# Performance work log

Hardware: AMD Instinct MI355X
Metric: run time of the kernel (lower is better)

## Reference

```python
import jax, jax.numpy as jnp
import numpy as np

N_VERTS = 100000
N_FACES = 200000
C = 512


def setup_inputs() -> dict:
    key = jax.random.key(0)
    ks = jax.random.split(key, 12)
    x = jax.random.normal(ks[0], (1, N_VERTS, C), dtype=jnp.float32) * 0.1
    verts = jax.random.normal(ks[1], (N_VERTS, 3), dtype=jnp.float32)
    faces = jax.random.randint(ks[2], (N_FACES, 3), 0, N_VERTS, dtype=jnp.int32)
    def lin(k, fan_in, fan_out):
        return jax.random.normal(k, (fan_in, fan_out), dtype=jnp.float32) / np.sqrt(fan_in)
    return {
        "x": x, "verts": verts, "faces": faces,
        "W1": lin(ks[3], C, C),    "b1": jnp.zeros((C,), jnp.float32),
        "W2": lin(ks[4], C, 512),  "b2": jnp.zeros((512,), jnp.float32),
        "W3": lin(ks[5], 512, 256),"b3": jnp.zeros((256,), jnp.float32),
        "W4": lin(ks[6], 256, 12), "b4": jnp.zeros((12,), jnp.float32),
    }


def special_procrustes(M):
    # roma.special_procrustes: nearest rotation in SO(3) to M, batched [F,3,3]
    U, S, Vh = jnp.linalg.svd(M)
    det = jnp.linalg.det(jnp.matmul(U, Vh))  # [F]
    D = jnp.stack([jnp.ones_like(det), jnp.ones_like(det), det], axis=-1)  # [F,3]
    return jnp.matmul(U * D[:, None, :], Vh)


def reference(x, verts, faces, W1, b1, W2, b2, W3, b3, W4, b4):
    N = verts.shape[0]
    F = faces.shape[0]
    # prism base: gather 3 vertex positions per face -> [F,3,3]
    prism_base = verts[faces]
    # gather features of the 3 face vertices and mean over them -> [F,C]
    feat = x[0][faces].mean(axis=1)
    # mlp_refine
    h = jax.nn.relu(feat @ W1 + b1)
    h = jax.nn.relu(h @ W2 + b2)
    h = jax.nn.relu(h @ W3 + b3)
    out = h @ W4 + b4  # [F,12]
    # batched 3x3 Procrustes rotation + translation
    rotations = special_procrustes(out[:, :9].reshape(F, 3, 3))
    translations = out[:, 9:]  # [F,3]
    transformed_prism = jnp.matmul(prism_base, rotations) + translations[:, None, :]  # [F,3,3]
    # scatter-add back to vertices with per-vertex face-count normalization
    flat_idx = faces.reshape(-1)  # [3F]
    summed = jax.ops.segment_sum(transformed_prism.reshape(-1, 3), flat_idx, num_segments=N)
    counts = jax.ops.segment_sum(jnp.ones((3 * F,), jnp.float32), flat_idx, num_segments=N)
    features = summed / jnp.clip(counts, 1.0)[:, None]  # [N,3]
    return features[None], transformed_prism, rotations
```

## Files before the change

### kernel.cpp

```cpp
#include <hip/hip_runtime.h>
#include <stdint.h>

typedef __attribute__((ext_vector_type(8))) short short8;
typedef __attribute__((ext_vector_type(4))) float f32x4;
typedef __attribute__((ext_vector_type(4))) unsigned short u16x4;

__device__ __forceinline__ unsigned short f2bf(float x) {
    union { float f; uint32_t u; } v; v.f = x;
    uint32_t u = v.u;
    uint32_t r = (u + 0x7FFFu + ((u >> 16) & 1u)) >> 16;
    return (unsigned short)r;
}
__device__ __forceinline__ float bf2f(unsigned short h) {
    union { uint32_t u; float f; } v; v.u = ((uint32_t)h) << 16;
    return v.f;
}
__device__ __forceinline__ void splitT(float f, unsigned short& hi, unsigned short& lo) {
    union { float f; uint32_t u; } a; a.f = f;
    hi = (unsigned short)(a.u >> 16);
    union { uint32_t u; float f; } b; b.u = a.u & 0xFFFF0000u;
    union { float f; uint32_t u; } c; c.f = f - b.f;
    lo = (unsigned short)(c.u >> 16);
}

__device__ __forceinline__ void gld_lds16(const void* g, void* s) {
    __builtin_amdgcn_global_load_lds(
        (const __attribute__((address_space(1))) void*)(uintptr_t)g,
        (__attribute__((address_space(3))) void*)(uint32_t)(uintptr_t)s,
        16, 0, 0);
}

__device__ __forceinline__ f32x4 mfma16(short8 a, short8 b, f32x4 c) {
    return __builtin_amdgcn_mfma_f32_16x16x32_bf16(a, b, c, 0, 0, 0);
}

__global__ void zero_kernel(float* __restrict__ sums, float* __restrict__ counts, int nverts) {
    int t = blockIdx.x * 256 + threadIdx.x;
    if (t < nverts * 3) sums[t] = 0.0f;
    if (t < nverts)     counts[t] = 0.0f;
}

__global__ void prep_weights(const float* __restrict__ W1, const float* __restrict__ W2,
                             const float* __restrict__ W3,
                             unsigned short* __restrict__ w1h, unsigned short* __restrict__ w1l,
                             unsigned short* __restrict__ w2h, unsigned short* __restrict__ w2l,
                             unsigned short* __restrict__ w3h, unsigned short* __restrict__ w3l) {
    int t = blockIdx.x * 256 + threadIdx.x;
    float v; unsigned short *ph, *pl; size_t o;
    if (t < 262144) {
        int k = t >> 9, n = t & 511;
        v = W1[t]; o = (size_t)n * 512 + k; ph = w1h; pl = w1l;
    } else if (t < 524288) {
        int u = t - 262144; int k = u >> 9, n = u & 511;
        v = W2[u]; o = (size_t)n * 512 + k; ph = w2h; pl = w2l;
    } else if (t < 655360) {
        int u = t - 524288; int k = u >> 8, n = u & 255;
        v = W3[u]; o = (size_t)n * 512 + k; ph = w3h; pl = w3l;
    } else return;
    unsigned short hi = f2bf(v);
    unsigned short lo = f2bf(v - bf2f(hi));
    ph[o] = hi; pl[o] = lo;
}

__global__ void gather_mean(const float* __restrict__ x, const int* __restrict__ faces,
                            unsigned short* __restrict__ Fhi, unsigned short* __restrict__ Flo,
                            int fbase, int fcount, int mrows) {
    int t = blockIdx.x * 256 + threadIdx.x;
    if (t >= (mrows << 7)) return;
    int r = t >> 7;
    int c = (t & 127) << 2;
    f32x4 m = {0.f, 0.f, 0.f, 0.f};
    if (r < fcount) {
        int f = fbase + r;
        int i0 = faces[3 * f], i1 = faces[3 * f + 1], i2 = faces[3 * f + 2];
        f32x4 a = *(const f32x4*)(x + (size_t)i0 * 512 + c);
        f32x4 b = *(const f32x4*)(x + (size_t)i1 * 512 + c);
        f32x4 d = *(const f32x4*)(x + (size_t)i2 * 512 + c);
        m = (a + b + d) * (1.0f / 3.0f);
    }
    u16x4 hv, lv;
#pragma unroll
    for (int j = 0; j < 4; ++j) {
        unsigned short hi = f2bf(m[j]);
        hv[j] = hi;
        lv[j] = f2bf(m[j] - bf2f(hi));
    }
    *(u16x4*)(Fhi + (size_t)r * 512 + c) = hv;
    *(u16x4*)(Flo + (size_t)r * 512 + c) = lv;
}

template<int OUT>
__global__ __launch_bounds__(256, 2)
void gemm_pipe(const unsigned short* __restrict__ Ahi, const unsigned short* __restrict__ Alo,
               const unsigned short* __restrict__ Bhi, const unsigned short* __restrict__ Blo,
               const float* __restrict__ bias,
               void* __restrict__ Out0, unsigned short* __restrict__ Olo,
               int N, int K, int nt) {
    __shared__ __align__(16) unsigned short sm[2][4][128 * 32];

    const int tid  = threadIdx.x;
    const int lane = tid & 63;
    const int w    = tid >> 6;
    const int wr = w >> 1, wc = w & 1;

    const int nwg  = gridDim.x;
    const int orig = blockIdx.x;
    const int q = nwg >> 3, r8 = nwg & 7;
    const int xcd = orig & 7, idx = orig >> 3;
    const int wg = (xcd < r8 ? xcd * (q + 1) : r8 * (q + 1) + (xcd - r8) * q) + idx;
    const int m0 = (wg / nt) << 7;
    const int n0 = (wg % nt) << 7;

    f32x4 acc[4][4] = {};

    const int s_lo  = w * 64 + lane;
    const int row0  = s_lo >> 2;
    const int c0    = ((s_lo & 3) - ((row0 >> 1) & 3)) & 3;
    const int s_hi  = 256 + s_lo;
    const int row1  = (s_hi >> 2) & 127;
    const int c1    = ((s_hi & 3) - ((row1 >> 1) & 3)) & 3;

    auto stage = [&](int b, int t) {
        const int k0 = t << 5;
        const unsigned short* const mats[4] = {Ahi, Alo, Bhi, Blo};
#pragma unroll
        for (int p = 0; p < 4; ++p) {
            const unsigned short* mat = mats[p];
            const int base0 = (p < 2) ? m0 : n0;
            gld_lds16(mat + (size_t)(base0 + row0) * K + (k0 + (c0 << 3)),
                      &sm[b][p][(w * 64) * 8]);
            gld_lds16(mat + (size_t)(base0 + row1) * K + (k0 + (c1 << 3)),
                      &sm[b][p][(256 + w * 64) * 8]);
        }
    };

    const int NT = K >> 5;
    stage(0, 0);
    stage(1, 1);

    const int kc  = lane >> 4;
    const int rbA = (wr << 6) + (lane & 15);
    const int rbB = (wc << 6) + (lane & 15);

    for (int t = 0; t < NT; ++t) {
        const int cur = t & 1;

        if (t + 1 < NT) asm volatile("s_waitcnt vmcnt(8)" ::: "memory");
        else            asm volatile("s_waitcnt vmcnt(0)" ::: "memory");
        __builtin_amdgcn_s_barrier();

        short8 ah[4], al[4], bh[4], bl[4];
#pragma unroll
        for (int m = 0; m < 4; ++m) {
            const int r   = rbA + (m << 4);
            const int off = r * 32 + (((kc + (r >> 1)) & 3) << 3);
            ah[m] = *(const short8*)&sm[cur][0][off];
            al[m] = *(const short8*)&sm[cur][1][off];
        }
#pragma unroll
        for (int n = 0; n < 4; ++n) {
            const int r   = rbB + (n << 4);
            const int off = r * 32 + (((kc + (r >> 1)) & 3) << 3);
            bh[n] = *(const short8*)&sm[cur][2][off];
            bl[n] = *(const short8*)&sm[cur][3][off];
        }
        asm volatile("s_waitcnt lgkmcnt(0)" ::: "memory");
        __builtin_amdgcn_sched_barrier(0);
        __builtin_amdgcn_s_barrier();

        if (t + 2 < NT) stage(cur, t + 2);

        __builtin_amdgcn_s_setprio(1);
#pragma unroll
        for (int m = 0; m < 4; ++m)
#pragma unroll
            for (int n = 0; n < 4; ++n)
                acc[m][n] = mfma16(ah[m], bh[n], acc[m][n]);
#pragma unroll
        for (int m = 0; m < 4; ++m)
#pragma unroll
            for (int n = 0; n < 4; ++n)
                acc[m][n] = mfma16(al[m], bh[n], acc[m][n]);
#pragma unroll
        for (int m = 0; m < 4; ++m)
#pragma unroll
            for (int n = 0; n < 4; ++n)
                acc[m][n] = mfma16(ah[m], bl[n], acc[m][n]);
        __builtin_amdgcn_s_setprio(0);
    }

#pragma unroll
    for (int n = 0; n < 4; ++n) {
        const int col = n0 + (wc << 6) + (n << 4) + (lane & 15);
        const float bv = (OUT == 1) ? 0.0f : bias[col];
#pragma unroll
        for (int m = 0; m < 4; ++m) {
            const int rbase = m0 + (wr << 6) + (m << 4) + ((lane >> 4) << 2);
#pragma unroll
            for (int j = 0; j < 4; ++j) {
                const size_t o = (size_t)(rbase + j) * N + col;
                if (OUT == 1) {
                    ((float*)Out0)[o] = acc[m][n][j];
                } else if (OUT == 2) {
                    ((float*)Out0)[o] = fmaxf(acc[m][n][j] + bv, 0.0f);
                } else {
                    float v = fmaxf(acc[m][n][j] + bv, 0.0f);
                    unsigned short hi = f2bf(v);
                    ((unsigned short*)Out0)[o] = hi;
                    Olo[o] = f2bf(v - bf2f(hi));
                }
            }
        }
    }
}

__global__ __launch_bounds__(256, 2)
void gemm_l1(const float* __restrict__ X,
             const unsigned short* __restrict__ Bhi, const unsigned short* __restrict__ Blo,
             float* __restrict__ Out,
             int N, int K, int nt, int nvalid) {
    __shared__ __align__(16) unsigned short sm[2][4][128 * 32];

    const int tid  = threadIdx.x;
    const int lane = tid & 63;
    const int w    = tid >> 6;
    const int wr = w >> 1, wc = w & 1;

    const int nwg  = gridDim.x;
    const int orig = blockIdx.x;
    const int q = nwg >> 3, r8 = nwg & 7;
    const int xcd = orig & 7, idx = orig >> 3;
    const int wg = (xcd < r8 ? xcd * (q + 1) : r8 * (q + 1) + (xcd - r8) * q) + idx;
    const int m0 = (wg / nt) << 7;
    const int n0 = (wg % nt) << 7;

    f32x4 acc[4][4] = {};

    int arow[2], achk[2], adst[2], avalid[2];
#pragma unroll
    for (int i = 0; i < 2; ++i) {
        const int s   = i * 256 + tid;
        const int row = s >> 2;
        const int c   = s & 3;
        arow[i]   = row;
        achk[i]   = c;
        adst[i]   = row * 32 + (((c + (row >> 1)) & 3) << 3);
        avalid[i] = (m0 + row) < nvalid;
    }
    const int s_lo  = w * 64 + lane;
    const int row0  = s_lo >> 2;
    const int c0    = ((s_lo & 3) - ((row0 >> 1) & 3)) & 3;
    const int s_hi  = 256 + s_lo;
    const int row1  = (s_hi >> 2) & 127;
    const int c1    = ((s_hi & 3) - ((row1 >> 1) & 3)) & 3;

    f32x4 fA[2][2];

    auto issueA = [&](int t) {
        const int k0 = t << 5;
#pragma unroll
        for (int i = 0; i < 2; ++i) {
            const int gr = avalid[i] ? (m0 + arow[i]) : 0;
            const float* src = X + (size_t)gr * K + (k0 + (achk[i] << 3));
            fA[i][0] = *(const f32x4*)src;
            fA[i][1] = *(const f32x4*)(src + 4);
        }
    };
    auto issueB = [&](int b, int t) {
        const int k0 = t << 5;
        gld_lds16(Bhi + (size_t)(n0 + row0) * K + (k0 + (c0 << 3)), &sm[b][2][(w * 64) * 8]);
        gld_lds16(Bhi + (size_t)(n0 + row1) * K + (k0 + (c1 << 3)), &sm[b][2][(256 + w * 64) * 8]);
        gld_lds16(Blo + (size_t)(n0 + row0) * K + (k0 + (c0 << 3)), &sm[b][3][(w * 64) * 8]);
        gld_lds16(Blo + (size_t)(n0 + row1) * K + (k0 + (c1 << 3)), &sm[b][3][(256 + w * 64) * 8]);
    };
    auto cvtWriteA = [&](int b) {
#pragma unroll
        for (int i = 0; i < 2; ++i) {
            short8 hv, lv;
#pragma unroll
            for (int j = 0; j < 8; ++j) {
                float f = avalid[i] ? fA[i][j >> 2][j & 3] : 0.0f;
                unsigned short hi, lo;
                splitT(f, hi, lo);
                hv[j] = (short)hi;
                lv[j] = (short)lo;
            }
            *(short8*)&sm[b][0][adst[i]] = hv;
            *(short8*)&sm[b][1][adst[i]] = lv;
        }
    };

    const int NT = K >> 5;
    issueA(0); issueB(0, 0);
    asm volatile("s_waitcnt vmcnt(4)" ::: "memory");
    cvtWriteA(0);
    issueA(1); issueB(1, 1);
    asm volatile("s_waitcnt vmcnt(4)" ::: "memory");
    cvtWriteA(1);
    asm volatile("s_waitcnt lgkmcnt(0)" ::: "memory");

    const int kc  = lane >> 4;
    const int rbA = (wr << 6) + (lane & 15);
    const int rbB = (wc << 6) + (lane & 15);

    for (int t = 0; t < NT; ++t) {
        const int cur = t & 1;

        if (t + 1 < NT) asm volatile("s_waitcnt vmcnt(4)" ::: "memory");
        else            asm volatile("s_waitcnt vmcnt(0)" ::: "memory");
        __builtin_amdgcn_s_barrier();

        short8 ah[4], al[4], bh[4], bl[4];
#pragma unroll
        for (int m = 0; m < 4; ++m) {
            const int r   = rbA + (m << 4);
            const int off = r * 32 + (((kc + (r >> 1)) & 3) << 3);
            ah[m] = *(const short8*)&sm[cur][0][off];
            al[m] = *(const short8*)&sm[cur][1][off];
        }
#pragma unroll
        for (int n = 0; n < 4; ++n) {
            const int r   = rbB + (n << 4);
            const int off = r * 32 + (((kc + (r >> 1)) & 3) << 3);
            bh[n] = *(const short8*)&sm[cur][2][off];
            bl[n] = *(const short8*)&sm[cur][3][off];
        }
        asm volatile("s_waitcnt lgkmcnt(0)" ::: "memory");
        __builtin_amdgcn_sched_barrier(0);
        __builtin_amdgcn_s_barrier();

        const int doStage = (t + 2 < NT);
        if (doStage) { issueA(t + 2); issueB(cur, t + 2); }

        __builtin_amdgcn_s_setprio(1);
#pragma unroll
        for (int m = 0; m < 4; ++m)
#pragma unroll
            for (int n = 0; n < 4; ++n)
                acc[m][n] = mfma16(ah[m], bh[n], acc[m][n]);
#pragma unroll
        for (int m = 0; m < 4; ++m)
#pragma unroll
            for (int n = 0; n < 4; ++n)
                acc[m][n] = mfma16(al[m], bh[n], acc[m][n]);
#pragma unroll
        for (int m = 0; m < 4; ++m)
#pragma unroll
            for (int n = 0; n < 4; ++n)
                acc[m][n] = mfma16(ah[m], bl[n], acc[m][n]);
        __builtin_amdgcn_s_setprio(0);

        if (doStage) {
            asm volatile("s_waitcnt vmcnt(4)" ::: "memory");
            cvtWriteA(cur);
        }
    }

#pragma unroll
    for (int n = 0; n < 4; ++n) {
        const int col = n0 + (wc << 6) + (n << 4) + (lane & 15);
#pragma unroll
        for (int m = 0; m < 4; ++m) {
            const int rbase = m0 + (wr << 6) + (m << 4) + ((lane >> 4) << 2);
#pragma unroll
            for (int j = 0; j < 4; ++j)
                Out[(size_t)(rbase + j) * N + col] = acc[m][n][j];
        }
    }
}

__global__ __launch_bounds__(256, 2)
void gemm_l2g(const float* __restrict__ Y, const int* __restrict__ faces,
              const float* __restrict__ b1,
              const unsigned short* __restrict__ Bhi, const unsigned short* __restrict__ Blo,
              const float* __restrict__ bias2,
              unsigned short* __restrict__ Ohi, unsigned short* __restrict__ Olo,
              int N, int K, int nt, int nvalid) {
    __shared__ __align__(16) unsigned short sm[2][4][128 * 32];

    const int tid  = threadIdx.x;
    const int lane = tid & 63;
    const int w    = tid >> 6;
    const int wr = w >> 1, wc = w & 1;

    const int nwg  = gridDim.x;
    const int orig = blockIdx.x;
    const int q = nwg >> 3, r8 = nwg & 7;
    const int xcd = orig & 7, idx = orig >> 3;
    const int wg = (xcd < r8 ? xcd * (q + 1) : r8 * (q + 1) + (xcd - r8) * q) + idx;
    const int m0 = (wg / nt) << 7;
    const int n0 = (wg % nt) << 7;

    f32x4 acc[4][4] = {};

    int adst[2], avalid[2];
    int fidx[2][3];
    const int achk = tid & 3;
#pragma unroll
    for (int i = 0; i < 2; ++i) {
        const int s   = i * 256 + tid;
        const int row = s >> 2;
        adst[i]   = row * 32 + (((achk + (row >> 1)) & 3) << 3);
        const int gf  = m0 + row;
        avalid[i] = gf < nvalid;
        const int gfs = avalid[i] ? gf : 0;
        fidx[i][0] = faces[3 * gfs];
        fidx[i][1] = faces[3 * gfs + 1];
        fidx[i][2] = faces[3 * gfs + 2];
    }
    const int s_lo  = w * 64 + lane;
    const int row0  = s_lo >> 2;
    const int c0    = ((s_lo & 3) - ((row0 >> 1) & 3)) & 3;
    const int s_hi  = 256 + s_lo;
    const int row1  = (s_hi >> 2) & 127;
    const int c1    = ((s_hi & 3) - ((row1 >> 1) & 3)) & 3;

    f32x4 fA[2][3][2];
    f32x4 fb[2];

    auto issueA = [&](int t) {
        const int koff = (t << 5) + (achk << 3);
#pragma unroll
        for (int i = 0; i < 2; ++i) {
#pragma unroll
            for (int r = 0; r < 3; ++r) {
                const float* src = Y + (size_t)fidx[i][r] * K + koff;
                fA[i][r][0] = *(const f32x4*)src;
                fA[i][r][1] = *(const f32x4*)(src + 4);
            }
        }
        fb[0] = *(const f32x4*)(b1 + koff);
        fb[1] = *(const f32x4*)(b1 + koff + 4);
    };
    auto issueB = [&](int b, int t) {
        const int k0 = t << 5;
        gld_lds16(Bhi + (size_t)(n0 + row0) * K + (k0 + (c0 << 3)), &sm[b][2][(w * 64) * 8]);
        gld_lds16(Bhi + (size_t)(n0 + row1) * K + (k0 + (c1 << 3)), &sm[b][2][(256 + w * 64) * 8]);
        gld_lds16(Blo + (size_t)(n0 + row0) * K + (k0 + (c0 << 3)), &sm[b][3][(w * 64) * 8]);
        gld_lds16(Blo + (size_t)(n0 + row1) * K + (k0 + (c1 << 3)), &sm[b][3][(256 + w * 64) * 8]);
    };
    auto cvtWriteA = [&](int b) {
        const float third = 1.0f / 3.0f;
#pragma unroll
        for (int i = 0; i < 2; ++i) {
            short8 hv, lv;
#pragma unroll
            for (int j = 0; j < 8; ++j) {
                const int h = j >> 2, e = j & 3;
                float f = 0.0f;
                if (avalid[i]) {
                    f = (fA[i][0][h][e] + fA[i][1][h][e] + fA[i][2][h][e]) * third + fb[h][e];
                    f = fmaxf(f, 0.0f);
                }
                unsigned short hi, lo;
                splitT(f, hi, lo);
                hv[j] = (short)hi;
                lv[j] = (short)lo;
            }
            *(short8*)&sm[b][0][adst[i]] = hv;
            *(short8*)&sm[b][1][adst[i]] = lv;
        }
    };

    const int NT = K >> 5;
    issueA(0); issueB(0, 0);
    asm volatile("s_waitcnt vmcnt(4)" ::: "memory");
    cvtWriteA(0);
    issueA(1); issueB(1, 1);
    asm volatile("s_waitcnt vmcnt(4)" ::: "memory");
    cvtWriteA(1);
    asm volatile("s_waitcnt lgkmcnt(0)" ::: "memory");

    const int kc  = lane >> 4;
    const int rbA = (wr << 6) + (lane & 15);
    const int rbB = (wc << 6) + (lane & 15);

    for (int t = 0; t < NT; ++t) {
        const int cur = t & 1;

        if (t + 1 < NT) asm volatile("s_waitcnt vmcnt(4)" ::: "memory");
        else            asm volatile("s_waitcnt vmcnt(0)" ::: "memory");
        __builtin_amdgcn_s_barrier();

        short8 ah[4], al[4], bh[4], bl[4];
#pragma unroll
        for (int m = 0; m < 4; ++m) {
            const int r   = rbA + (m << 4);
            const int off = r * 32 + (((kc + (r >> 1)) & 3) << 3);
            ah[m] = *(const short8*)&sm[cur][0][off];
            al[m] = *(const short8*)&sm[cur][1][off];
        }
#pragma unroll
        for (int n = 0; n < 4; ++n) {
            const int r   = rbB + (n << 4);
            const int off = r * 32 + (((kc + (r >> 1)) & 3) << 3);
            bh[n] = *(const short8*)&sm[cur][2][off];
            bl[n] = *(const short8*)&sm[cur][3][off];
        }
        asm volatile("s_waitcnt lgkmcnt(0)" ::: "memory");
        __builtin_amdgcn_sched_barrier(0);
        __builtin_amdgcn_s_barrier();

        const int doStage = (t + 2 < NT);
        if (doStage) { issueA(t + 2); issueB(cur, t + 2); }

        __builtin_amdgcn_s_setprio(1);
#pragma unroll
        for (int m = 0; m < 4; ++m)
#pragma unroll
            for (int n = 0; n < 4; ++n)
                acc[m][n] = mfma16(ah[m], bh[n], acc[m][n]);
#pragma unroll
        for (int m = 0; m < 4; ++m)
#pragma unroll
            for (int n = 0; n < 4; ++n)
                acc[m][n] = mfma16(al[m], bh[n], acc[m][n]);
#pragma unroll
        for (int m = 0; m < 4; ++m)
#pragma unroll
            for (int n = 0; n < 4; ++n)
                acc[m][n] = mfma16(ah[m], bl[n], acc[m][n]);
        __builtin_amdgcn_s_setprio(0);

        if (doStage) {
            asm volatile("s_waitcnt vmcnt(4)" ::: "memory");
            cvtWriteA(cur);
        }
    }

#pragma unroll
    for (int n = 0; n < 4; ++n) {
        const int col = n0 + (wc << 6) + (n << 4) + (lane & 15);
        const float bv = bias2[col];
#pragma unroll
        for (int m = 0; m < 4; ++m) {
            const int rbase = m0 + (wr << 6) + (m << 4) + ((lane >> 4) << 2);
#pragma unroll
            for (int j = 0; j < 4; ++j) {
                const size_t o = (size_t)(rbase + j) * N + col;
                float v = fmaxf(acc[m][n][j] + bv, 0.0f);
                unsigned short hi, lo;
                splitT(v, hi, lo);
                __builtin_nontemporal_store(hi, Ohi + o);
                __builtin_nontemporal_store(lo, Olo + o);
            }
        }
    }
}

#define JROT(app, aqq, apq, apz, aqz, vp0, vp1, vp2, vq0, vq1, vq2) do {          \
    float _apq = (apq);                                                            \
    if (fabsf(_apq) > 1e-30f) {                                                    \
        float _tau = ((aqq) - (app)) / (2.0f * _apq);                              \
        float _t = copysignf(1.0f, _tau) / (fabsf(_tau) + sqrtf(1.0f + _tau*_tau));\
        float _c = 1.0f / sqrtf(1.0f + _t*_t);                                     \
        float _s = _t * _c;                                                        \
        (app) = (app) - _t * _apq;                                                 \
        (aqq) = (aqq) + _t * _apq;                                                 \
        (apq) = 0.0f;                                                              \
        float _pz = (apz), _qz = (aqz);                                            \
        (apz) = _c * _pz - _s * _qz;                                               \
        (aqz) = _s * _pz + _c * _qz;                                               \
        float _x;                                                                  \
        _x = (vp0); (vp0) = _c*_x - _s*(vq0); (vq0) = _s*_x + _c*(vq0);            \
        _x = (vp1); (vp1) = _c*_x - _s*(vq1); (vq1) = _s*_x + _c*(vq1);            \
        _x = (vp2); (vp2) = _c*_x - _s*(vq2); (vq2) = _s*_x + _c*(vq2);            \
    }                                                                              \
} while (0)

#define SWAP3(la, lb, x0, y0, z0, x1, y1, z1) do {                \
    float _tm;                                                    \
    _tm = la; la = lb; lb = _tm;                                  \
    _tm = x0; x0 = x1; x1 = _tm;                                  \
    _tm = y0; y0 = y1; y1 = _tm;                                  \
    _tm = z0; z0 = z1; z1 = _tm;                                  \
} while (0)

__global__ void face_kernel(const float* __restrict__ H3,
                            const float* __restrict__ W4, const float* __restrict__ b4,
                            const float* __restrict__ verts, const int* __restrict__ faces,
                            float* __restrict__ out_tp, float* __restrict__ out_rot,
                            float* __restrict__ sums, float* __restrict__ counts,
                            int fbase, int fcount) {
    __shared__ float sW[256 * 12 + 12];
    for (int i = threadIdx.x; i < 256 * 12 + 12; i += 256)
        sW[i] = (i < 256 * 12) ? W4[i] : b4[i - 256 * 12];
    __syncthreads();

    const int r = blockIdx.x * 256 + threadIdx.x;
    if (r >= fcount) return;
    const int f = fbase + r;

    float o[12];
#pragma unroll
    for (int n = 0; n < 12; ++n) o[n] = sW[3072 + n];
    const f32x4* ph = (const f32x4*)(H3 + (size_t)r * 256);
    for (int kb = 0; kb < 64; ++kb) {
        f32x4 hv = ph[kb];
#pragma unroll
        for (int kk = 0; kk < 4; ++kk) {
            float val = hv[kk];
            const float* wrow = &sW[(kb * 4 + kk) * 12];
#pragma unroll
            for (int n = 0; n < 12; ++n) o[n] = fmaf(val, wrow[n], o[n]);
        }
    }

    const float M00=o[0], M01=o[1], M02=o[2];
    const float M10=o[3], M11=o[4], M12=o[5];
    const float M20=o[6], M21=o[7], M22=o[8];
    const float t0 =o[9], t1 =o[10], t2 =o[11];

    float a00 = M00*M00 + M10*M10 + M20*M20;
    float a11 = M01*M01 + M11*M11 + M21*M21;
    float a22 = M02*M02 + M12*M12 + M22*M22;
    float a01 = M00*M01 + M10*M11 + M20*M21;
    float a02 = M00*M02 + M10*M12 + M20*M22;
    float a12 = M01*M02 + M11*M12 + M21*M22;

    float v00=1.f, v01=0.f, v02=0.f;
    float v10=0.f, v11=1.f, v12=0.f;
    float v20=0.f, v21=0.f, v22=1.f;
#pragma unroll
    for (int sweep = 0; sweep < 5; ++sweep) {
        JROT(a00, a11, a01, a02, a12, v00, v10, v20, v01, v11, v21);
        JROT(a00, a22, a02, a01, a12, v00, v10, v20, v02, v12, v22);
        JROT(a11, a22, a12, a01, a02, v01, v11, v21, v02, v12, v22);
    }
    float l0 = a00, l1 = a11, l2 = a22;
    if (l0 < l1) SWAP3(l0, l1, v00, v10, v20, v01, v11, v21);
    if (l0 < l2) SWAP3(l0, l2, v00, v10, v20, v02, v12, v22);
    if (l1 < l2) SWAP3(l1, l2, v01, v11, v21, v02, v12, v22);

    float b1x = M00*v00 + M01*v10 + M02*v20;
    float b1y = M10*v00 + M11*v10 + M12*v20;
    float b1z = M20*v00 + M21*v10 + M22*v20;
    float b2x = M00*v01 + M01*v11 + M02*v21;
    float b2y = M10*v01 + M11*v11 + M12*v21;
    float b2z = M20*v01 + M21*v11 + M22*v21;

    float n1 = sqrtf(b1x*b1x + b1y*b1y + b1z*b1z);
    float u1x, u1y, u1z;
    if (n1 > 1e-25f) { float in = 1.0f / n1; u1x = b1x*in; u1y = b1y*in; u1z = b1z*in; }
    else             { u1x = 1.f; u1y = 0.f; u1z = 0.f; }

    float dp  = b2x*u1x + b2y*u1y + b2z*u1z;
    float w2x = b2x - dp*u1x, w2y = b2y - dp*u1y, w2z = b2z - dp*u1z;
    float n2  = sqrtf(w2x*w2x + w2y*w2y + w2z*w2z);
    float u2x, u2y, u2z;
    if (n2 > 1e-25f) { float in = 1.0f / n2; u2x = w2x*in; u2y = w2y*in; u2z = w2z*in; }
    else {
        float ex = (fabsf(u1x) < 0.9f) ? 1.f : 0.f;
        float ey = 1.f - ex;
        float cx = -u1z * ey, cy = u1z * ex, cz = u1x * ey - u1y * ex;
        float cn = rsqrtf(cx*cx + cy*cy + cz*cz);
        u2x = cx * cn; u2y = cy * cn; u2z = cz * cn;
    }
    float u3x = u1y*u2z - u1z*u2y;
    float u3y = u1z*u2x - u1x*u2z;
    float u3z = u1x*u2y - u1y*u2x;

    float dv = v00*(v11*v22 - v12*v21) - v01*(v10*v22 - v12*v20) + v02*(v10*v21 - v11*v20);
    if (dv < 0.f) { v02 = -v02; v12 = -v12; v22 = -v22; }

    float R00 = u1x*v00 + u2x*v01 + u3x*v02;
    float R01 = u1x*v10 + u2x*v11 + u3x*v12;
    float R02 = u1x*v20 + u2x*v21 + u3x*v22;
    float R10 = u1y*v00 + u2y*v01 + u3y*v02;
    float R11 = u1y*v10 + u2y*v11 + u3y*v12;
    float R12 = u1y*v20 + u2y*v21 + u3y*v22;
    float R20 = u1z*v00 + u2z*v01 + u3z*v02;
    float R21 = u1z*v10 + u2z*v11 + u3z*v12;
    float R22 = u1z*v20 + u2z*v21 + u3z*v22;

    float* rp = out_rot + (size_t)f * 9;
    rp[0]=R00; rp[1]=R01; rp[2]=R02;
    rp[3]=R10; rp[4]=R11; rp[5]=R12;
    rp[6]=R20; rp[7]=R21; rp[8]=R22;

    float* tp = out_tp + (size_t)f * 9;
    const int idx[3] = { faces[3*f], faces[3*f+1], faces[3*f+2] };
#pragma unroll
    for (int j = 0; j < 3; ++j) {
        const int vi = idx[j];
        float px = verts[3*vi], py = verts[3*vi+1], pz = verts[3*vi+2];
        float q0 = px*R00 + py*R10 + pz*R20 + t0;
        float q1 = px*R01 + py*R11 + pz*R21 + t1;
        float q2 = px*R02 + py*R12 + pz*R22 + t2;
        tp[j*3+0] = q0; tp[j*3+1] = q1; tp[j*3+2] = q2;
        atomicAdd(&sums[(size_t)vi*3+0], q0);
        atomicAdd(&sums[(size_t)vi*3+1], q1);
        atomicAdd(&sums[(size_t)vi*3+2], q2);
        atomicAdd(&counts[vi], 1.0f);
    }
}

__global__ void finalize_kernel(float* __restrict__ feats, const float* __restrict__ counts, int nverts) {
    int v = blockIdx.x * 256 + threadIdx.x;
    if (v >= nverts) return;
    float c = fmaxf(counts[v], 1.0f);
    feats[v*3+0] = feats[v*3+0] / c;
    feats[v*3+1] = feats[v*3+1] / c;
    feats[v*3+2] = feats[v*3+2] / c;
}

extern "C" void kernel_launch(void* const* d_in, const int* in_sizes, int n_in,
                              void* d_out, int out_size, void* d_ws, size_t ws_size,
                              hipStream_t stream) {
    const float* x     = (const float*)d_in[0];
    const float* verts = (const float*)d_in[1];
    const int*   faces = (const int*)d_in[2];
    const float* W1 = (const float*)d_in[3];
    const float* b1 = (const float*)d_in[4];
    const float* W2 = (const float*)d_in[5];
    const float* b2 = (const float*)d_in[6];
    const float* W3 = (const float*)d_in[7];
    const float* b3 = (const float*)d_in[8];
    const float* W4 = (const float*)d_in[9];
    const float* b4 = (const float*)d_in[10];

    const int nverts = in_sizes[1] / 3;
    const int nfaces = in_sizes[2] / 3;

    float* out_feats = (float*)d_out;
    float* out_tp    = out_feats + (size_t)nverts * 3;
    float* out_rot   = out_tp + (size_t)nfaces * 9;

    char* ws = (char*)d_ws;
    size_t cur = 0;
    auto carve = [&](size_t bytes) -> void* {
        void* p = ws + cur;
        cur += (bytes + 255) & ~(size_t)255;
        return p;
    };
    unsigned short* w1h = (unsigned short*)carve(512 * 512 * 2);
    unsigned short* w1l = (unsigned short*)carve(512 * 512 * 2);
    unsigned short* w2h = (unsigned short*)carve(512 * 512 * 2);
    unsigned short* w2l = (unsigned short*)carve(512 * 512 * 2);
    unsigned short* w3h = (unsigned short*)carve(256 * 512 * 2);
    unsigned short* w3l = (unsigned short*)carve(256 * 512 * 2);
    float* counts = (float*)carve((size_t)nverts * 4);

    const long MV = ((long)nverts + 127) & ~127L;
    const long MF = ((long)nfaces + 127) & ~127L;
    const size_t szY   = (size_t)MV * 512 * 4;
    const size_t szH2w = (size_t)MF * 512 * 2;
    const size_t szH3f = (size_t)MF * 256 * 4;

    const size_t sR1 = (szY > szH3f) ? szY : szH3f;
    const size_t sR2 = szH2w;
    const size_t sR3 = szH2w;
    const size_t need = cur + sR1 + sR2 + sR3 + 4 * 256;

    zero_kernel<<<(nverts * 3 + 255) / 256, 256, 0, stream>>>(out_feats, counts, nverts);
    prep_weights<<<(655360 + 255) / 256, 256, 0, stream>>>(W1, W2, W3, w1h, w1l, w2h, w2l, w3h, w3l);

    if (ws_size >= need) {
        char* R1 = (char*)carve(sR1);
        char* R2 = (char*)carve(sR2);
        char* R3 = (char*)carve(sR3);
        float*          y   = (float*)R1;
        float*          h3  = (float*)R1;
        unsigned short* h2h = (unsigned short*)R2;
        unsigned short* h2l = (unsigned short*)R3;

        gemm_l1<<<(int)(MV / 128) * 4, 256, 0, stream>>>(x, w1h, w1l, y, 512, 512, 4, nverts);

        gemm_l2g<<<(int)(MF / 128) * 4, 256, 0, stream>>>(y, faces, b1, w2h, w2l, b2,
                                                          h2h, h2l, 512, 512, 4, nfaces);

        gemm_pipe<2><<<(int)(MF / 128) * 2, 256, 0, stream>>>(h2h, h2l, w3h, w3l, b3, h3, nullptr, 256, 512, 2);

        face_kernel<<<(nfaces + 255) / 256, 256, 0, stream>>>(h3, W4, b4, verts, faces,
                                                              out_tp, out_rot, out_feats, counts,
                                                              0, nfaces);
    } else {
        long mpad = MF;
        size_t avail = (ws_size > cur) ? (ws_size - cur) : 0;
        long chp = (long)(avail / 4096);
        chp &= ~127L;
        if (chp > mpad) chp = mpad;
        if (chp < 128) chp = 128;
        unsigned short* bAh = (unsigned short*)carve((size_t)chp * 512 * 2);
        unsigned short* bAl = (unsigned short*)carve((size_t)chp * 512 * 2);
        unsigned short* bBh = (unsigned short*)carve((size_t)chp * 512 * 2);
        unsigned short* bBl = (unsigned short*)carve((size_t)chp * 512 * 2);

        for (long base = 0; base < nfaces; base += chp) {
            long rem = (long)nfaces - base;
            int cnt = (int)((rem < chp) ? rem : chp);
            int mc  = (cnt + 127) & ~127;

            gather_mean<<<mc / 2, 256, 0, stream>>>(x, faces, bAh, bAl, (int)base, cnt, mc);
            gemm_pipe<0><<<(mc / 128) * 4, 256, 0, stream>>>(bAh, bAl, w1h, w1l, b1, bBh, bBl, 512, 512, 4);
            gemm_pipe<0><<<(mc / 128) * 4, 256, 0, stream>>>(bBh, bBl, w2h, w2l, b2, bAh, bAl, 512, 512, 4);
            gemm_pipe<2><<<(mc / 128) * 2, 256, 0, stream>>>(bAh, bAl, w3h, w3l, b3, (float*)bBh, nullptr, 256, 512, 2);
            face_kernel<<<(cnt + 255) / 256, 256, 0, stream>>>((float*)bBh, W4, b4, verts, faces,
                                                               out_tp, out_rot, out_feats, counts,
                                                               (int)base, cnt);
        }
    }

    finalize_kernel<<<(nverts + 255) / 256, 256, 0, stream>>>(out_feats, counts, nverts);
}
```

Before: 1.236 ms.

## Prefetch gathered A tiles one stage earlier with double register buffers

In gemm_l2g, the gathered vertex-feature loads for the A operand are now issued one K-tile further ahead, using two alternating register buffers (fA0/fA1). The vmcnt waits are adjusted so the MFMA loop only waits on the LDS-staged data it needs. This is meant to hide the latency of the irregular global gathers behind more compute. In exchange it roughly doubles the registers holding staged A data, which risks spills or lower occupancy under launch_bounds(256,2). The output stores also change from nontemporal to ordinary stores.

```diff
diff --git a/kernel.cpp b/kernel.cpp
--- a/kernel.cpp
+++ b/kernel.cpp
@@ -369,6 +369,43 @@
     }
 }
 
+#define L2G_ISSUEA(FA, FB, t) do {                                          \
+    const int koff_ = ((t) << 5) + (achk << 3);                             \
+    _Pragma("unroll")                                                       \
+    for (int i_ = 0; i_ < 2; ++i_) {                                        \
+        _Pragma("unroll")                                                   \
+        for (int r_ = 0; r_ < 3; ++r_) {                                    \
+            const float* src_ = Y + (size_t)fidx[i_][r_] * K + koff_;       \
+            FA[i_][r_][0] = *(const f32x4*)src_;                            \
+            FA[i_][r_][1] = *(const f32x4*)(src_ + 4);                      \
+        }                                                                   \
+    }                                                                       \
+    FB[0] = *(const f32x4*)(b1 + koff_);                                    \
+    FB[1] = *(const f32x4*)(b1 + koff_ + 4);                                \
+} while (0)
+
+#define L2G_CVTW(FA, FB, b) do {                                            \
+    _Pragma("unroll")                                                       \
+    for (int i_ = 0; i_ < 2; ++i_) {                                        \
+        short8 hv_, lv_;                                                    \
+        _Pragma("unroll")                                                   \
+        for (int j_ = 0; j_ < 8; ++j_) {                                    \
+            const int h_ = j_ >> 2, e_ = j_ & 3;                            \
+            float f_ = 0.0f;                                                \
+            if (avalid[i_]) {                                               \
+                f_ = (FA[i_][0][h_][e_] + FA[i_][1][h_][e_] +               \
+                      FA[i_][2][h_][e_]) * (1.0f / 3.0f) + FB[h_][e_];      \
+                f_ = fmaxf(f_, 0.0f);                                       \
+            }                                                               \
+            unsigned short hi_, lo_;                                        \
+            splitT(f_, hi_, lo_);                                           \
+            hv_[j_] = (short)hi_; lv_[j_] = (short)lo_;                     \
+        }                                                                   \
+        *(short8*)&sm[b][0][adst[i_]] = hv_;                                \
+        *(short8*)&sm[b][1][adst[i_]] = lv_;                                \
+    }                                                                       \
+} while (0)
+
 __global__ __launch_bounds__(256, 2)
 void gemm_l2g(const float* __restrict__ Y, const int* __restrict__ faces,
               const float* __restrict__ b1,
@@ -415,23 +452,9 @@
     const int row1  = (s_hi >> 2) & 127;
     const int c1    = ((s_hi & 3) - ((row1 >> 1) & 3)) & 3;
 
-    f32x4 fA[2][3][2];
-    f32x4 fb[2];
-
-    auto issueA = [&](int t) {
-        const int koff = (t << 5) + (achk << 3);
-#pragma unroll
-        for (int i = 0; i < 2; ++i) {
-#pragma unroll
-            for (int r = 0; r < 3; ++r) {
-                const float* src = Y + (size_t)fidx[i][r] * K + koff;
-                fA[i][r][0] = *(const f32x4*)src;
-                fA[i][r][1] = *(const f32x4*)(src + 4);
-            }
-        }
-        fb[0] = *(const f32x4*)(b1 + koff);
-        fb[1] = *(const f32x4*)(b1 + koff + 4);
-    };
+    f32x4 fA0[2][3][2], fA1[2][3][2];
+    f32x4 fb0[2], fb1[2];
+
     auto issueB = [&](int b, int t) {
         const int k0 = t << 5;
         gld_lds16(Bhi + (size_t)(n0 + row0) * K + (k0 + (c0 << 3)), &sm[b][2][(w * 64) * 8]);
@@ -439,36 +462,15 @@
         gld_lds16(Blo + (size_t)(n0 + row0) * K + (k0 + (c0 << 3)), &sm[b][3][(w * 64) * 8]);
         gld_lds16(Blo + (size_t)(n0 + row1) * K + (k0 + (c1 << 3)), &sm[b][3][(256 + w * 64) * 8]);
     };
-    auto cvtWriteA = [&](int b) {
-        const float third = 1.0f / 3.0f;
-#pragma unroll
-        for (int i = 0; i < 2; ++i) {
-            short8 hv, lv;
-#pragma unroll
-            for (int j = 0; j < 8; ++j) {
-                const int h = j >> 2, e = j & 3;
-                float f = 0.0f;
-                if (avalid[i]) {
-                    f = (fA[i][0][h][e] + fA[i][1][h][e] + fA[i][2][h][e]) * third + fb[h][e];
-                    f = fmaxf(f, 0.0f);
-                }
-                unsigned short hi, lo;
-                splitT(f, hi, lo);
-                hv[j] = (short)hi;
-                lv[j] = (short)lo;
-            }
-            *(short8*)&sm[b][0][adst[i]] = hv;
-            *(short8*)&sm[b][1][adst[i]] = lv;
-        }
-    };
 
     const int NT = K >> 5;
-    issueA(0); issueB(0, 0);
+    L2G_ISSUEA(fA0, fb0, 0); issueB(0, 0);
     asm volatile("s_waitcnt vmcnt(4)" ::: "memory");
-    cvtWriteA(0);
-    issueA(1); issueB(1, 1);
+    L2G_CVTW(fA0, fb0, 0);
+    L2G_ISSUEA(fA1, fb1, 1); issueB(1, 1);
     asm volatile("s_waitcnt vmcnt(4)" ::: "memory");
-    cvtWriteA(1);
+    L2G_CVTW(fA1, fb1, 1);
+    L2G_ISSUEA(fA0, fb0, 2);
     asm volatile("s_waitcnt lgkmcnt(0)" ::: "memory");
 
     const int kc  = lane >> 4;
@@ -478,8 +480,9 @@
     for (int t = 0; t < NT; ++t) {
         const int cur = t & 1;
 
-        if (t + 1 < NT) asm volatile("s_waitcnt vmcnt(4)" ::: "memory");
-        else            asm volatile("s_waitcnt vmcnt(0)" ::: "memory");
+        if (t + 2 < NT)      asm volatile("s_waitcnt vmcnt(18)" ::: "memory");
+        else if (t + 1 < NT) asm volatile("s_waitcnt vmcnt(4)" ::: "memory");
+        else                 asm volatile("s_waitcnt vmcnt(0)" ::: "memory");
         __builtin_amdgcn_s_barrier();
 
         short8 ah[4], al[4], bh[4], bl[4];
@@ -501,8 +504,7 @@
         __builtin_amdgcn_sched_barrier(0);
         __builtin_amdgcn_s_barrier();
 
-        const int doStage = (t + 2 < NT);
-        if (doStage) { issueA(t + 2); issueB(cur, t + 2); }
+        if (t + 2 < NT) issueB(cur, t + 2);
 
         __builtin_amdgcn_s_setprio(1);
 #pragma unroll
@@ -522,9 +524,14 @@
                 acc[m][n] = mfma16(ah[m], bl[n], acc[m][n]);
         __builtin_amdgcn_s_setprio(0);
 
-        if (doStage) {
+        if (t + 2 < NT) {
             asm volatile("s_waitcnt vmcnt(4)" ::: "memory");
-            cvtWriteA(cur);
+            if (cur == 0) L2G_CVTW(fA0, fb0, 0);
+            else          L2G_CVTW(fA1, fb1, 1);
+        }
+        if (t + 3 < NT) {
+            if (cur == 0) L2G_ISSUEA(fA1, fb1, t + 3);
+            else          L2G_ISSUEA(fA0, fb0, t + 3);
         }
     }
 
@@ -541,8 +548,8 @@
                 float v = fmaxf(acc[m][n][j] + bv, 0.0f);
                 unsigned short hi, lo;
                 splitT(v, hi, lo);
-                __builtin_nontemporal_store(hi, Ohi + o);
-                __builtin_nontemporal_store(lo, Olo + o);
+                Ohi[o] = hi;
+                Olo[o] = lo;
             }
         }
     }
```

After: 1.636 ms. 1.32x slower.
